# Kernel tuning notes

Measured on AMD Instinct MI355X. Metric: run time of the kernel, lower is better.

## Reference

```python
import jax, jax.numpy as jnp
import numpy as np

B, N, T, D, E, M = 8, 512, 64, 128, 32, 3


def _norm(v):
    return v / jnp.clip(jnp.linalg.norm(v, axis=-1, keepdims=True), 1e-12)


def setup_inputs() -> dict:
    key = jax.random.key(0)
    ks = jax.random.split(key, 14)
    s = 0.05
    x = jax.random.normal(ks[0], (B, N, T, 1), jnp.float32)
    # set_prior: binarized adjacency + self loops, row-normalized
    a = (jax.random.uniform(ks[1], (N, N)) > 0.95).astype(jnp.float32) + jnp.eye(N, dtype=jnp.float32)
    prior = a / jnp.clip(a.sum(1, keepdims=True), 1e-8)
    # orthogonal queries, as in torch __init__ (QR of zero-padded randn)
    rng = np.random.default_rng(0)
    qs = []
    for _ in range(M):
        pad = np.zeros((D, D), np.float32)
        pad[:E] = rng.standard_normal((E, D)).astype(np.float32) * 0.1
        q, _ = np.linalg.qr(pad)
        qs.append(q[:E])
    return {
        "x": x,
        "prior": prior,
        "proj_W": jax.random.normal(ks[2], (D, 1), jnp.float32) * s,
        "proj_b": jnp.zeros((D,), jnp.float32),
        "W_ih": jax.random.normal(ks[3], (3 * D, D), jnp.float32) * s,
        "W_hh": jax.random.normal(ks[4], (3 * D, D), jnp.float32) * s,
        "b_ih": jnp.zeros((3 * D,), jnp.float32),
        "b_hh": jnp.zeros((3 * D,), jnp.float32),
        "space_W": jax.random.normal(ks[5], (M, D, D), jnp.float32) * s,
        "space_b": jnp.zeros((M, D), jnp.float32),
        "router_W": jax.random.normal(ks[6], (M, 2 * D), jnp.float32) * s,
        "router_b": jnp.zeros((M,), jnp.float32),
        "out_W": jax.random.normal(ks[7], (1, D), jnp.float32) * s,
        "out_b": jnp.zeros((1,), jnp.float32),
        "prior_logit": jnp.array(1.0, jnp.float32),
        "queries": jnp.asarray(np.stack(qs)),  # [M, E, D]
    }


def reference(x, prior, proj_W, proj_b, W_ih, W_hh, b_ih, b_hh,
              space_W, space_b, router_W, router_b, out_W, out_b,
              prior_logit, queries):
    b, n, t, _ = x.shape
    d = proj_b.shape[0]
    m, e, _ = queries.shape
    # proj(x.permute(0,2,1,3)).reshape(B*N, T, D)  (faithful reshape of [B,T,N,D])
    hp = jnp.transpose(x, (0, 2, 1, 3)) @ proj_W.T + proj_b  # [B,T,N,D]
    seq = hp.reshape(b * n, t, d)
    xs = jnp.swapaxes(seq, 0, 1)  # [T, BN, D]

    def gru_step(h, xt):
        gi = xt @ W_ih.T + b_ih
        gh = h @ W_hh.T + b_hh
        ir, iz, i_n = jnp.split(gi, 3, axis=-1)
        hr, hz, h_n = jnp.split(gh, 3, axis=-1)
        r = jax.nn.sigmoid(ir + hr)
        z = jax.nn.sigmoid(iz + hz)
        ng = jnp.tanh(i_n + r * h_n)
        return (1.0 - z) * ng + z * h, None

    h, _ = jax.lax.scan(gru_step, jnp.zeros((b * n, d), x.dtype), xs)
    h = h.reshape(b, n, d)

    stats = jnp.concatenate([h.mean(1), jnp.std(h, axis=1, ddof=1)], axis=-1)  # torch std is unbiased
    probs = jax.nn.softmax(stats @ router_W.T + router_b, axis=-1)  # [B,M]

    z_prior = jnp.einsum('ij,bjd->bid', prior, h)

    hs = _norm(jnp.einsum('bnd,mkd->bmnk', h, space_W) + space_b[None, :, None, :])  # [B,M,N,D]
    q = _norm(queries)  # [M,E,D]
    scores = jnp.einsum('bmnd,med->bmen', hs, q)  # [B,M,E,N] (topk over N axis)
    k = min(n, max(4, int(n * 0.05)))
    vals, idx = jax.lax.top_k(scores, k)  # [B,M,E,k]
    w = jax.nn.softmax(vals / 0.7, axis=-1)
    H = jnp.zeros((b, m, e, n), h.dtype).at[
        jnp.arange(b)[:, None, None, None],
        jnp.arange(m)[None, :, None, None],
        jnp.arange(e)[None, None, :, None],
        idx,
    ].set(w)  # [B,M,E,N], transposed layout of torch's [B,N,E]

    Hmix = jnp.einsum('bmen,bm->ben', H, probs)  # [B,E,N] == torch Hmix^T
    edge = jnp.einsum('ben,bnd->bed', Hmix, h)   # Hmix^T @ h
    z_learn = jnp.einsum('ben,bed->bnd', Hmix, edge)  # Hmix @ edge

    alpha = jax.nn.sigmoid(prior_logit)
    out = (alpha * z_prior + (1.0 - alpha) * z_learn) @ out_W.T + out_b  # [B,N,1]
    return out.squeeze(-1), probs
```

## Files before the change

kernel.cpp:

```cpp
#include <hip/hip_runtime.h>
#include <math.h>

#define OFF_U      0
#define OFF_C      384
#define OFF_QWHI   768
#define OFF_QWLO   6912
#define OFF_H      13056
#define OFF_PROBS  537344
#define OFF_HV     537376
#define OFF_SCORES 541472
#define OFF_HMIX   934688
#define OFF_WHI    1066016
#define OFF_SHI    1115168
#define OFF_SLO    1139744
#define OFF_STATS  1164320
#define OFF_EV     1229856
#define OFF_QB     1230112

#define L2E_F 1.44269504088896340736f

typedef short bf16x8 __attribute__((ext_vector_type(8)));
typedef float f32x4 __attribute__((ext_vector_type(4)));

union U8 { unsigned short s[8]; bf16x8 v; uint4 u4; };

__device__ __forceinline__ unsigned short bf16_rtn(float f) {
  unsigned int u = __float_as_uint(f);
  return (unsigned short)((u + 0x7FFFu + ((u >> 16) & 1u)) >> 16);
}
__device__ __forceinline__ float bf16_f(unsigned short h) {
  return __uint_as_float(((unsigned int)h) << 16);
}

__global__ __launch_bounds__(256) void prep_kernel(const float* __restrict__ Wih,
                                                   const float* __restrict__ projW,
                                                   const float* __restrict__ projb,
                                                   const float* __restrict__ bih,
                                                   const float* __restrict__ queries,
                                                   const float* __restrict__ Whh,
                                                   const float* __restrict__ spaceW,
                                                   const float* __restrict__ spaceb,
                                                   float* __restrict__ ws) {
  const int bid = blockIdx.x, tid = threadIdx.x;
  const int wave = tid >> 6, lane = tid & 63;
  if (bid < 96) {
    int r = bid * 4 + wave;
    float w0 = Wih[r * 128 + lane], w1 = Wih[r * 128 + 64 + lane];
    float u = w0 * projW[lane] + w1 * projW[64 + lane];
    float c = w0 * projb[lane] + w1 * projb[64 + lane];
    for (int off = 32; off; off >>= 1) {
      u += __shfl_xor(u, off);
      c += __shfl_xor(c, off);
    }
    if (lane == 0) {
      ws[OFF_U + r] = u;
      ws[OFF_C + r] = c + bih[r];
    }
  } else if (bid < 112) {
    unsigned short* WHI = (unsigned short*)(ws + OFF_WHI);
    int base = (bid - 96) * 3072;
    for (int i = tid; i < 3072; i += 256) {
      int idx = base + i;
      float sc = (idx < 32768) ? L2E_F : (2.f * L2E_F);
      WHI[idx] = bf16_rtn(Whh[idx] * sc);
    }
  } else if (bid < 128) {
    unsigned short* SHI = (unsigned short*)(ws + OFF_SHI);
    unsigned short* SLO = (unsigned short*)(ws + OFF_SLO);
    int base = (bid - 112) * 3072;
    for (int i = tid; i < 3072; i += 256) {
      float w = spaceW[base + i];
      unsigned short hi = bf16_rtn(w);
      SHI[base + i] = hi;
      SLO[base + i] = bf16_rtn(w - bf16_f(hi));
    }
  } else if (bid < 224) {
    int qi = bid - 128;
    int m = qi >> 5, e = qi & 31;
    __shared__ float invS, qdS;
    const float* qrow = queries + (m * 32 + e) * 128;
    if (wave == 0) {
      float v0 = qrow[lane], v1 = qrow[64 + lane];
      float ss = v0 * v0 + v1 * v1;
      for (int off = 32; off; off >>= 1) ss += __shfl_xor(ss, off);
      if (lane == 0) invS = 1.f / fmaxf(sqrtf(ss), 1e-12f);
    } else if (wave == 1) {
      float v = qrow[lane] * spaceb[m * 128 + lane] +
                qrow[64 + lane] * spaceb[m * 128 + 64 + lane];
      for (int off = 32; off; off >>= 1) v += __shfl_xor(v, off);
      if (lane == 0) qdS = v;
    }
    __syncthreads();
    if (tid < 128) {
      int din = tid;
      float acc = 0.f;
      for (int dout = 0; dout < 128; ++dout)
        acc += qrow[dout] * spaceW[m * 16384 + dout * 128 + din];
      acc *= invS;
      unsigned short hi = bf16_rtn(acc);
      ((unsigned short*)(ws + OFF_QWHI))[(m * 32 + e) * 128 + din] = hi;
      ((unsigned short*)(ws + OFF_QWLO))[(m * 32 + e) * 128 + din] =
          bf16_rtn(acc - bf16_f(hi));
    }
    if (tid == 255) ws[OFF_QB + m * 32 + e] = qdS * invS;
  } else {
    ws[OFF_EV + tid] = 0.f;
  }
}

#define GRU_STEP(RB, WB, T)                                                         \
  do {                                                                              \
    f32x4 acc0 = c0i, acc1 = c1i, acc2 = c2i;                                       \
    _Pragma("unroll") for (int c = 0; c < 4; ++c) {                                 \
      bf16x8 Bf = *(const bf16x8*)&hB[RB][rdOff + c * 32];                          \
      acc0 = __builtin_amdgcn_mfma_f32_16x16x32_bf16(Ah[0][c], Bf, acc0, 0, 0, 0);  \
      acc1 = __builtin_amdgcn_mfma_f32_16x16x32_bf16(Ah[1][c], Bf, acc1, 0, 0, 0);  \
      acc2 = __builtin_amdgcn_mfma_f32_16x16x32_bf16(Ah[2][c], Bf, acc2, 0, 0, 0);  \
    }                                                                               \
    const float xsv = xsAll[xsOff + (T)];                                           \
    float hv[4];                                                                    \
    _Pragma("unroll") for (int r = 0; r < 4; ++r) {                                 \
      float gr = fmaf(xsv, ur[r], acc0[r]);                                         \
      float gz = fmaf(xsv, uz[r], acc1[r]);                                         \
      float gn = fmaf(xsv, un[r], cnv[r]);                                          \
      float rr = __builtin_amdgcn_rcpf(1.f + __builtin_amdgcn_exp2f(-gr));          \
      float zm = __builtin_amdgcn_rcpf(1.f + __builtin_amdgcn_exp2f(gz));           \
      float a = fmaf(rr, acc2[r], gn);                                              \
      float ng = fmaf(-2.f, __builtin_amdgcn_rcpf(__builtin_amdgcn_exp2f(a) + 1.f), \
                      1.f);                                                         \
      hv[r] = fmaf(zm, ng - hreg[r], hreg[r]);                                      \
      hreg[r] = hv[r];                                                              \
    }                                                                               \
    unsigned int pk0, pk1;                                                          \
    asm("v_cvt_pk_bf16_f32 %0, %1, %2" : "=v"(pk0) : "v"(hv[0]), "v"(hv[1]));       \
    asm("v_cvt_pk_bf16_f32 %0, %1, %2" : "=v"(pk1) : "v"(hv[2]), "v"(hv[3]));       \
    *(uint2*)&hB[WB][wrOff] = make_uint2(pk0, pk1);                                 \
    __syncthreads();                                                                \
  } while (0)

__global__ __launch_bounds__(512, 2) void gru_kernel(const float* __restrict__ x,
                                                     const float* __restrict__ bhh,
                                                     const float* __restrict__ outW,
                                                     float* __restrict__ ws) {
  __shared__ __align__(16) unsigned short hB[2][16 * 136];
  __shared__ float xsAll[16 * 65];
  __shared__ float hFin[16 * 132];

  const int tid = threadIdx.x, wave = tid >> 6, lane = tid & 63;
  const int q = lane >> 4, s15 = lane & 15;
  const int d0 = wave * 16 + q * 4;
  const unsigned short* WHI = (const unsigned short*)(ws + OFF_WHI);

  {
    float4 z4 = make_float4(0.f, 0.f, 0.f, 0.f);
    float4* hm4 = (float4*)(ws + OFF_HMIX);
    if (tid < 128) hm4[blockIdx.x * 128 + tid] = z4;
  }

  bf16x8 Ah[3][4];
#pragma unroll
  for (int t = 0; t < 3; ++t) {
    int row = (wave + 8 * t) * 16 + s15;
#pragma unroll
    for (int c = 0; c < 4; ++c)
      Ah[t][c] = *(const bf16x8*)&WHI[row * 128 + c * 32 + q * 8];
  }

  float ur[4], uz[4], un[4], cnv[4];
  f32x4 c0i, c1i, c2i;
#pragma unroll
  for (int r = 0; r < 4; ++r) {
    int d = d0 + r;
    ur[r] = ws[OFF_U + d] * L2E_F;
    uz[r] = ws[OFF_U + 128 + d] * L2E_F;
    un[r] = ws[OFF_U + 256 + d] * (2.f * L2E_F);
    c0i[r] = (ws[OFF_C + d] + bhh[d]) * L2E_F;
    c1i[r] = (ws[OFF_C + 128 + d] + bhh[128 + d]) * L2E_F;
    cnv[r] = ws[OFF_C + 256 + d] * (2.f * L2E_F);
    c2i[r] = bhh[256 + d] * (2.f * L2E_F);
  }

  const int seq0 = blockIdx.x * 16;
  for (int i = tid; i < 1024; i += 512) {
    int s = i >> 6, tt = i & 63;
    int r = (seq0 + s) * 64 + tt;
    xsAll[s * 65 + tt] = x[((r >> 15) * 512 + (r & 511)) * 64 + ((r >> 9) & 63)];
  }
  for (int i = tid; i < 2176; i += 512) hB[0][i] = 0;
  __syncthreads();

  float hreg[4] = {0.f, 0.f, 0.f, 0.f};
  const int rdOff = s15 * 136 + q * 8;
  const int wrOff = s15 * 136 + d0;
  const int xsOff = s15 * 65;

#pragma unroll 1
  for (int t2 = 0; t2 < 32; ++t2) {
    GRU_STEP(0, 1, 2 * t2);
    GRU_STEP(1, 0, 2 * t2 + 1);
  }

#pragma unroll
  for (int r = 0; r < 4; ++r) hFin[s15 * 132 + d0 + r] = hreg[r];
  __syncthreads();
  float* h_out = ws + OFF_H;
#pragma unroll
  for (int p = 0; p < 4; ++p) {
    int item = tid + p * 512;
    int s = item >> 7, dd = item & 127;
    h_out[(seq0 + s) * 128 + dd] = hFin[s * 132 + dd];
  }
  for (int s = wave * 2; s < wave * 2 + 2; ++s) {
    float a = hFin[s * 132 + lane] * outW[lane] + hFin[s * 132 + 64 + lane] * outW[64 + lane];
    for (int off = 32; off; off >>= 1) a += __shfl_xor(a, off);
    if (lane == 0) ws[OFF_HV + seq0 + s] = a;
  }
  if (tid < 128) {
    float s = 0.f, q2 = 0.f;
#pragma unroll
    for (int sI = 0; sI < 16; ++sI) {
      float v = hFin[sI * 132 + tid];
      s += v; q2 += v * v;
    }
    ws[OFF_STATS + blockIdx.x * 256 + tid] = s;
    ws[OFF_STATS + blockIdx.x * 256 + 128 + tid] = q2;
  }
}

__global__ __launch_bounds__(256) void scores_kernel(const float* __restrict__ spaceb,
                                                     const float* __restrict__ routerW,
                                                     const float* __restrict__ routerb,
                                                     float* __restrict__ ws,
                                                     float* __restrict__ d_out) {
  const int bid = blockIdx.x;
  const int chunk = bid & 15, m = (bid >> 4) % 3, b = bid / 48;
  const int n0 = chunk * 32;
  const int tid = threadIdx.x, wave = tid >> 6, lane = tid & 63;
  const int q = lane >> 4, s15 = lane & 15;

  __shared__ __align__(16) unsigned short sHi[16 * 33 * 8];
  __shared__ __align__(16) unsigned short sLo[16 * 33 * 8];
  __shared__ float hsL[32 * 132];
  __shared__ float biasL[128];
  __shared__ float invnL[32];
  __shared__ float qbL[32];

  const float* hG = ws + OFF_H;
  const unsigned short* SHI = (const unsigned short*)(ws + OFF_SHI);
  const unsigned short* SLO = (const unsigned short*)(ws + OFF_SLO);
  const unsigned short* QWHI = (const unsigned short*)(ws + OFF_QWHI);
  const unsigned short* QWLO = (const unsigned short*)(ws + OFF_QWLO);

  if (tid < 128) biasL[tid] = spaceb[m * 128 + tid];
  else if (tid < 160) qbL[tid - 128] = ws[OFF_QB + m * 32 + (tid - 128)];
  {
    int nn = tid >> 3, kc = tid & 7;
    const float* row = &hG[(b * 512 + n0 + nn) * 128 + kc * 16];
    U8 ph0, pl0, ph1, pl1;
#pragma unroll
    for (int j = 0; j < 8; ++j) {
      float v = row[j];
      unsigned short hi = bf16_rtn(v);
      ph0.s[j] = hi; pl0.s[j] = bf16_rtn(v - bf16_f(hi));
    }
#pragma unroll
    for (int j = 0; j < 8; ++j) {
      float v = row[8 + j];
      unsigned short hi = bf16_rtn(v);
      ph1.s[j] = hi; pl1.s[j] = bf16_rtn(v - bf16_f(hi));
    }
    int g0 = kc * 2;
    *(uint4*)&sHi[(g0 * 33 + nn) * 8] = ph0.u4;
    *(uint4*)&sLo[(g0 * 33 + nn) * 8] = pl0.u4;
    *(uint4*)&sHi[((g0 + 1) * 33 + nn) * 8] = ph1.u4;
    *(uint4*)&sLo[((g0 + 1) * 33 + nn) * 8] = pl1.u4;
  }
  __syncthreads();

  const int nt = wave >> 1;
  const int half = wave & 1;
  const int dt0 = half * 4;
  f32x4 acc[4] = {{0.f,0.f,0.f,0.f},{0.f,0.f,0.f,0.f},{0.f,0.f,0.f,0.f},{0.f,0.f,0.f,0.f}};
  f32x4 accS = {0.f, 0.f, 0.f, 0.f};
#pragma unroll
  for (int c = 0; c < 4; ++c) {
    bf16x8 Ahi = *(const bf16x8*)&sHi[((c * 4 + q) * 33 + nt * 16 + s15) * 8];
    bf16x8 Alo = *(const bf16x8*)&sLo[((c * 4 + q) * 33 + nt * 16 + s15) * 8];
#pragma unroll
    for (int i = 0; i < 4; ++i) {
      int row = m * 16384 + ((dt0 + i) * 16 + s15) * 128 + c * 32 + q * 8;
      bf16x8 Bhi = *(const bf16x8*)&SHI[row];
      bf16x8 Blo = *(const bf16x8*)&SLO[row];
      acc[i] = __builtin_amdgcn_mfma_f32_16x16x32_bf16(Ahi, Bhi, acc[i], 0, 0, 0);
      acc[i] = __builtin_amdgcn_mfma_f32_16x16x32_bf16(Alo, Bhi, acc[i], 0, 0, 0);
      acc[i] = __builtin_amdgcn_mfma_f32_16x16x32_bf16(Ahi, Blo, acc[i], 0, 0, 0);
    }
    {
      int row = (m * 32 + half * 16 + s15) * 128 + c * 32 + q * 8;
      bf16x8 Qhi = *(const bf16x8*)&QWHI[row];
      bf16x8 Qlo = *(const bf16x8*)&QWLO[row];
      accS = __builtin_amdgcn_mfma_f32_16x16x32_bf16(Ahi, Qhi, accS, 0, 0, 0);
      accS = __builtin_amdgcn_mfma_f32_16x16x32_bf16(Alo, Qhi, accS, 0, 0, 0);
      accS = __builtin_amdgcn_mfma_f32_16x16x32_bf16(Ahi, Qlo, accS, 0, 0, 0);
    }
  }
#pragma unroll
  for (int i = 0; i < 4; ++i) {
    int dcol = (dt0 + i) * 16 + s15;
    float bb = biasL[dcol];
#pragma unroll
    for (int r = 0; r < 4; ++r)
      hsL[(nt * 16 + q * 4 + r) * 132 + dcol] = acc[i][r] + bb;
  }
  __syncthreads();

  {
    int n = tid >> 3, kc = tid & 7;
    float ss = 0.f;
#pragma unroll
    for (int d4 = 0; d4 < 4; ++d4) {
      float4 v = *(const float4*)&hsL[n * 132 + kc * 16 + d4 * 4];
      ss += v.x * v.x + v.y * v.y + v.z * v.z + v.w * v.w;
    }
    ss += __shfl_xor(ss, 1); ss += __shfl_xor(ss, 2); ss += __shfl_xor(ss, 4);
    if (kc == 0) invnL[n] = 1.f / fmaxf(sqrtf(ss), 1e-12f);
  }
  __syncthreads();

  {
    int e = half * 16 + s15;
    float qb = qbL[e];
    int nb = nt * 16 + q * 4;
    float4 o;
    o.x = (accS[0] + qb) * invnL[nb + 0];
    o.y = (accS[1] + qb) * invnL[nb + 1];
    o.z = (accS[2] + qb) * invnL[nb + 2];
    o.w = (accS[3] + qb) * invnL[nb + 3];
    *(float4*)&ws[OFF_SCORES + ((b * 3 + m) * 32 + e) * 512 + n0 + nb] = o;
  }

  if ((bid % 48) == 0) {
    __syncthreads();
    float* st = hsL;
    float* lgS = hsL + 256;
    if (tid < 128) {
      float s = 0.f, q2 = 0.f;
      const float* base = ws + OFF_STATS + b * 32 * 256;
      for (int j = 0; j < 32; ++j) {
        s += base[j * 256 + tid];
        q2 += base[j * 256 + 128 + tid];
      }
      float mean = s * (1.f / 512.f);
      float var = (q2 - 512.f * mean * mean) * (1.f / 511.f);
      st[tid] = mean;
      st[128 + tid] = sqrtf(fmaxf(var, 0.f));
    }
    __syncthreads();
    if (tid < 3) {
      float acc2 = routerb[tid];
      for (int k = 0; k < 256; ++k) acc2 += st[k] * routerW[tid * 256 + k];
      lgS[tid] = acc2;
    }
    __syncthreads();
    if (tid == 0) {
      float mx = fmaxf(lgS[0], fmaxf(lgS[1], lgS[2]));
      float e0 = expf(lgS[0] - mx), e1 = expf(lgS[1] - mx), e2 = expf(lgS[2] - mx);
      float inv = 1.f / (e0 + e1 + e2);
      ws[OFF_PROBS + b * 3 + 0] = e0 * inv;
      ws[OFF_PROBS + b * 3 + 1] = e1 * inv;
      ws[OFF_PROBS + b * 3 + 2] = e2 * inv;
      d_out[4096 + b * 3 + 0] = e0 * inv;
      d_out[4096 + b * 3 + 1] = e1 * inv;
      d_out[4096 + b * 3 + 2] = e2 * inv;
    }
  }
}

__global__ __launch_bounds__(256) void topk_kernel(float* __restrict__ ws) {
  const int row0 = blockIdx.x * 4;
  const int b = row0 / 96;
  const int tid = threadIdx.x, wave = tid >> 6, lane = tid & 63;
  __shared__ float hvL[512];
  hvL[tid] = ws[OFF_HV + b * 512 + tid];
  hvL[256 + tid] = ws[OFF_HV + b * 512 + 256 + tid];
  __syncthreads();

  int row = row0 + wave;
  int m = (row / 32) % 3, e = row & 31;
  const float* sc = ws + OFF_SCORES + row * 512;
  float prob = ws[OFF_PROBS + b * 3 + m];

  float v[8];
#pragma unroll
  for (int j = 0; j < 8; ++j) v[j] = sc[j * 64 + lane];

  float selv = 0.f; int seli = 0; float maxv = 0.f;
  for (int it = 0; it < 25; ++it) {
    float bv = v[0]; int bj = 0;
#pragma unroll
    for (int j = 1; j < 8; ++j)
      if (v[j] > bv) { bv = v[j]; bj = j; }
    int bidx = bj * 64 + lane;
    for (int off = 32; off; off >>= 1) {
      float ov = __shfl_xor(bv, off);
      int oi = __shfl_xor(bidx, off);
      if (ov > bv || (ov == bv && oi < bidx)) { bv = ov; bidx = oi; }
    }
    if (lane == (bidx & 63)) v[bidx >> 6] = -INFINITY;
    if (it == 0) maxv = bv;
    if (lane == it) { selv = bv; seli = bidx; }
  }
  float ex = (lane < 25) ? __expf((selv - maxv) * (1.f / 0.7f)) : 0.f;
  float den = ex;
  for (int off = 32; off; off >>= 1) den += __shfl_xor(den, off);
  float w = prob * ex / den;
  if (lane < 25)
    atomicAdd(&ws[OFF_HMIX + (b * 32 + e) * 512 + seli], w);
  float evc = (lane < 25) ? w * hvL[seli] : 0.f;
  for (int off = 32; off; off >>= 1) evc += __shfl_xor(evc, off);
  if (lane == 0) atomicAdd(&ws[OFF_EV + b * 32 + e], evc);
}

__global__ __launch_bounds__(512) void final_kernel(const float* __restrict__ prior,
                                                    const float* __restrict__ outb,
                                                    const float* __restrict__ plog,
                                                    float* __restrict__ ws,
                                                    float* __restrict__ d_out) {
  const int bid = blockIdx.x;
  const int b = bid >> 4, ch = bid & 15;
  const int tid = threadIdx.x, wave = tid >> 6, lane = tid & 63;
  __shared__ float hvL[512], evL[32];
  hvL[tid] = ws[OFF_HV + b * 512 + tid];
  if (tid < 32) evL[tid] = ws[OFF_EV + b * 32 + tid];
  __syncthreads();
  float alpha = 1.f / (1.f + expf(-plog[0]));
  float ob = outb[0];
#pragma unroll
  for (int i = 0; i < 4; ++i) {
    int n = ch * 32 + wave * 4 + i;
    const float* pr = prior + n * 512;
    float s1 = 0.f;
#pragma unroll
    for (int j = 0; j < 8; ++j) s1 += pr[j * 64 + lane] * hvL[j * 64 + lane];
    float s2 = 0.f;
    if (lane < 32) s2 = ws[OFF_HMIX + (b * 32 + lane) * 512 + n] * evL[lane];
    float a = alpha * s1 + (1.f - alpha) * s2;
    for (int off = 32; off; off >>= 1) a += __shfl_xor(a, off);
    if (lane == 0) d_out[b * 512 + n] = a + ob;
  }
}

extern "C" void kernel_launch(void* const* d_in, const int* in_sizes, int n_in,
                              void* d_out, int out_size, void* d_ws, size_t ws_size,
                              hipStream_t stream) {
  const float* x       = (const float*)d_in[0];
  const float* prior   = (const float*)d_in[1];
  const float* projW   = (const float*)d_in[2];
  const float* projb   = (const float*)d_in[3];
  const float* Wih     = (const float*)d_in[4];
  const float* Whh     = (const float*)d_in[5];
  const float* bih     = (const float*)d_in[6];
  const float* bhh     = (const float*)d_in[7];
  const float* spaceW  = (const float*)d_in[8];
  const float* spaceb  = (const float*)d_in[9];
  const float* routerW = (const float*)d_in[10];
  const float* routerb = (const float*)d_in[11];
  const float* outW    = (const float*)d_in[12];
  const float* outb    = (const float*)d_in[13];
  const float* plog    = (const float*)d_in[14];
  const float* queries = (const float*)d_in[15];
  float* ws  = (float*)d_ws;
  float* out = (float*)d_out;

  prep_kernel<<<225, 256, 0, stream>>>(Wih, projW, projb, bih, queries, Whh,
                                       spaceW, spaceb, ws);
  gru_kernel<<<256, 512, 0, stream>>>(x, bhh, outW, ws);
  scores_kernel<<<384, 256, 0, stream>>>(spaceb, routerW, routerb, ws, out);
  topk_kernel<<<192, 256, 0, stream>>>(ws);
  final_kernel<<<128, 512, 0, stream>>>(prior, outb, plog, ws, out);
}
```

Baseline: 167.1 us.

## Halve GRU block to 4 waves, each computing two 16-row tiles per step

The GRU kernel now runs with 256 threads (4 waves) instead of 512, and each wave handles two 16-column slices of the hidden state. It loads B fragments from LDS once per step and reuses them across both tiles. The aim is to cut barrier cost per recurrent step and the redundant LDS reads of h. In exchange each wave carries twice the register state (W_hh fragments, accumulators, constants) and runs a longer serial chain of MFMA and gate math per step, so the per-step critical path may grow.

```diff
diff --git a/kernel.cpp b/kernel.cpp
--- a/kernel.cpp
+++ b/kernel.cpp
@@ -108,37 +108,50 @@
   }
 }
 
-#define GRU_STEP(RB, WB, T)                                                         \
+#define GRU_MFMA3(G, a0, a1, a2)                                                    \
+  _Pragma("unroll") for (int c = 0; c < 4; ++c) {                                   \
+    a0 = __builtin_amdgcn_mfma_f32_16x16x32_bf16(Ah[0][G][c], Bf[c], a0, 0, 0, 0);  \
+    a1 = __builtin_amdgcn_mfma_f32_16x16x32_bf16(Ah[1][G][c], Bf[c], a1, 0, 0, 0);  \
+    a2 = __builtin_amdgcn_mfma_f32_16x16x32_bf16(Ah[2][G][c], Bf[c], a2, 0, 0, 0);  \
+  }
+
+#define GRU_GATES(WB, a0, a1, a2, UR, UZ, UN, CNV, HR, WOFF)                        \
   do {                                                                              \
-    f32x4 acc0 = c0i, acc1 = c1i, acc2 = c2i;                                       \
-    _Pragma("unroll") for (int c = 0; c < 4; ++c) {                                 \
-      bf16x8 Bf = *(const bf16x8*)&hB[RB][rdOff + c * 32];                          \
-      acc0 = __builtin_amdgcn_mfma_f32_16x16x32_bf16(Ah[0][c], Bf, acc0, 0, 0, 0);  \
-      acc1 = __builtin_amdgcn_mfma_f32_16x16x32_bf16(Ah[1][c], Bf, acc1, 0, 0, 0);  \
-      acc2 = __builtin_amdgcn_mfma_f32_16x16x32_bf16(Ah[2][c], Bf, acc2, 0, 0, 0);  \
-    }                                                                               \
-    const float xsv = xsAll[xsOff + (T)];                                           \
     float hv[4];                                                                    \
     _Pragma("unroll") for (int r = 0; r < 4; ++r) {                                 \
-      float gr = fmaf(xsv, ur[r], acc0[r]);                                         \
-      float gz = fmaf(xsv, uz[r], acc1[r]);                                         \
-      float gn = fmaf(xsv, un[r], cnv[r]);                                          \
+      float gr = fmaf(xsv, UR[r], a0[r]);                                           \
+      float gz = fmaf(xsv, UZ[r], a1[r]);                                           \
+      float gn = fmaf(xsv, UN[r], CNV[r]);                                          \
       float rr = __builtin_amdgcn_rcpf(1.f + __builtin_amdgcn_exp2f(-gr));          \
       float zm = __builtin_amdgcn_rcpf(1.f + __builtin_amdgcn_exp2f(gz));           \
-      float a = fmaf(rr, acc2[r], gn);                                              \
+      float a = fmaf(rr, a2[r], gn);                                                \
       float ng = fmaf(-2.f, __builtin_amdgcn_rcpf(__builtin_amdgcn_exp2f(a) + 1.f), \
                       1.f);                                                         \
-      hv[r] = fmaf(zm, ng - hreg[r], hreg[r]);                                      \
-      hreg[r] = hv[r];                                                              \
+      hv[r] = fmaf(zm, ng - HR[r], HR[r]);                                          \
+      HR[r] = hv[r];                                                                \
     }                                                                               \
     unsigned int pk0, pk1;                                                          \
     asm("v_cvt_pk_bf16_f32 %0, %1, %2" : "=v"(pk0) : "v"(hv[0]), "v"(hv[1]));       \
     asm("v_cvt_pk_bf16_f32 %0, %1, %2" : "=v"(pk1) : "v"(hv[2]), "v"(hv[3]));       \
-    *(uint2*)&hB[WB][wrOff] = make_uint2(pk0, pk1);                                 \
+    *(uint2*)&hB[WB][WOFF] = make_uint2(pk0, pk1);                                  \
+  } while (0)
+
+#define GRU_STEP(RB, WB, T)                                                         \
+  do {                                                                              \
+    f32x4 a0A = c0iA, a1A = c1iA, a2A = c2iA;                                       \
+    f32x4 a0B = c0iB, a1B = c1iB, a2B = c2iB;                                       \
+    bf16x8 Bf[4];                                                                   \
+    _Pragma("unroll") for (int c = 0; c < 4; ++c)                                   \
+      Bf[c] = *(const bf16x8*)&hB[RB][rdOff + c * 32];                              \
+    const float xsv = xsAll[xsOff + (T)];                                           \
+    GRU_MFMA3(0, a0A, a1A, a2A)                                                     \
+    GRU_GATES(WB, a0A, a1A, a2A, urA, uzA, unA, cnvA, hA, wrA);                     \
+    GRU_MFMA3(1, a0B, a1B, a2B)                                                     \
+    GRU_GATES(WB, a0B, a1B, a2B, urB, uzB, unB, cnvB, hBr, wrB);                    \
     __syncthreads();                                                                \
   } while (0)
 
-__global__ __launch_bounds__(512, 2) void gru_kernel(const float* __restrict__ x,
+__global__ __launch_bounds__(256, 1) void gru_kernel(const float* __restrict__ x,
                                                      const float* __restrict__ bhh,
                                                      const float* __restrict__ outW,
                                                      float* __restrict__ ws) {
@@ -148,7 +161,8 @@
 
   const int tid = threadIdx.x, wave = tid >> 6, lane = tid & 63;
   const int q = lane >> 4, s15 = lane & 15;
-  const int d0 = wave * 16 + q * 4;
+  const int dA = wave * 32 + q * 4;
+  const int dB = dA + 16;
   const unsigned short* WHI = (const unsigned short*)(ws + OFF_WHI);
 
   {
@@ -157,41 +171,53 @@
     if (tid < 128) hm4[blockIdx.x * 128 + tid] = z4;
   }
 
-  bf16x8 Ah[3][4];
-#pragma unroll
-  for (int t = 0; t < 3; ++t) {
-    int row = (wave + 8 * t) * 16 + s15;
-#pragma unroll
-    for (int c = 0; c < 4; ++c)
-      Ah[t][c] = *(const bf16x8*)&WHI[row * 128 + c * 32 + q * 8];
-  }
-
-  float ur[4], uz[4], un[4], cnv[4];
-  f32x4 c0i, c1i, c2i;
+  bf16x8 Ah[3][2][4];
+#pragma unroll
+  for (int g = 0; g < 3; ++g)
+#pragma unroll
+    for (int T = 0; T < 2; ++T) {
+      int row = g * 128 + wave * 32 + T * 16 + s15;
+#pragma unroll
+      for (int c = 0; c < 4; ++c)
+        Ah[g][T][c] = *(const bf16x8*)&WHI[row * 128 + c * 32 + q * 8];
+    }
+
+  float urA[4], uzA[4], unA[4], cnvA[4], urB[4], uzB[4], unB[4], cnvB[4];
+  f32x4 c0iA, c1iA, c2iA, c0iB, c1iB, c2iB;
 #pragma unroll
   for (int r = 0; r < 4; ++r) {
-    int d = d0 + r;
-    ur[r] = ws[OFF_U + d] * L2E_F;
-    uz[r] = ws[OFF_U + 128 + d] * L2E_F;
-    un[r] = ws[OFF_U + 256 + d] * (2.f * L2E_F);
-    c0i[r] = (ws[OFF_C + d] + bhh[d]) * L2E_F;
-    c1i[r] = (ws[OFF_C + 128 + d] + bhh[128 + d]) * L2E_F;
-    cnv[r] = ws[OFF_C + 256 + d] * (2.f * L2E_F);
-    c2i[r] = bhh[256 + d] * (2.f * L2E_F);
+    int d = dA + r;
+    urA[r] = ws[OFF_U + d] * L2E_F;
+    uzA[r] = ws[OFF_U + 128 + d] * L2E_F;
+    unA[r] = ws[OFF_U + 256 + d] * (2.f * L2E_F);
+    c0iA[r] = (ws[OFF_C + d] + bhh[d]) * L2E_F;
+    c1iA[r] = (ws[OFF_C + 128 + d] + bhh[128 + d]) * L2E_F;
+    cnvA[r] = ws[OFF_C + 256 + d] * (2.f * L2E_F);
+    c2iA[r] = bhh[256 + d] * (2.f * L2E_F);
+    d = dB + r;
+    urB[r] = ws[OFF_U + d] * L2E_F;
+    uzB[r] = ws[OFF_U + 128 + d] * L2E_F;
+    unB[r] = ws[OFF_U + 256 + d] * (2.f * L2E_F);
+    c0iB[r] = (ws[OFF_C + d] + bhh[d]) * L2E_F;
+    c1iB[r] = (ws[OFF_C + 128 + d] + bhh[128 + d]) * L2E_F;
+    cnvB[r] = ws[OFF_C + 256 + d] * (2.f * L2E_F);
+    c2iB[r] = bhh[256 + d] * (2.f * L2E_F);
   }
 
   const int seq0 = blockIdx.x * 16;
-  for (int i = tid; i < 1024; i += 512) {
+  for (int i = tid; i < 1024; i += 256) {
     int s = i >> 6, tt = i & 63;
     int r = (seq0 + s) * 64 + tt;
     xsAll[s * 65 + tt] = x[((r >> 15) * 512 + (r & 511)) * 64 + ((r >> 9) & 63)];
   }
-  for (int i = tid; i < 2176; i += 512) hB[0][i] = 0;
-  __syncthreads();
-
-  float hreg[4] = {0.f, 0.f, 0.f, 0.f};
+  for (int i = tid; i < 2176; i += 256) hB[0][i] = 0;
+  __syncthreads();
+
+  float hA[4] = {0.f, 0.f, 0.f, 0.f};
+  float hBr[4] = {0.f, 0.f, 0.f, 0.f};
   const int rdOff = s15 * 136 + q * 8;
-  const int wrOff = s15 * 136 + d0;
+  const int wrA = s15 * 136 + dA;
+  const int wrB = s15 * 136 + dB;
   const int xsOff = s15 * 65;
 
 #pragma unroll 1
@@ -201,16 +227,19 @@
   }
 
 #pragma unroll
-  for (int r = 0; r < 4; ++r) hFin[s15 * 132 + d0 + r] = hreg[r];
+  for (int r = 0; r < 4; ++r) {
+    hFin[s15 * 132 + dA + r] = hA[r];
+    hFin[s15 * 132 + dB + r] = hBr[r];
+  }
   __syncthreads();
   float* h_out = ws + OFF_H;
 #pragma unroll
-  for (int p = 0; p < 4; ++p) {
-    int item = tid + p * 512;
+  for (int p = 0; p < 8; ++p) {
+    int item = tid + p * 256;
     int s = item >> 7, dd = item & 127;
     h_out[(seq0 + s) * 128 + dd] = hFin[s * 132 + dd];
   }
-  for (int s = wave * 2; s < wave * 2 + 2; ++s) {
+  for (int s = wave * 4; s < wave * 4 + 4; ++s) {
     float a = hFin[s * 132 + lane] * outW[lane] + hFin[s * 132 + 64 + lane] * outW[64 + lane];
     for (int off = 32; off; off >>= 1) a += __shfl_xor(a, off);
     if (lane == 0) ws[OFF_HV + seq0 + s] = a;
@@ -474,7 +503,7 @@
 
   prep_kernel<<<225, 256, 0, stream>>>(Wih, projW, projb, bih, queries, Whh,
                                        spaceW, spaceb, ws);
-  gru_kernel<<<256, 512, 0, stream>>>(x, bhh, outW, ws);
+  gru_kernel<<<256, 256, 0, stream>>>(x, bhh, outW, ws);
   scores_kernel<<<384, 256, 0, stream>>>(spaceb, routerW, routerb, ws, out);
   topk_kernel<<<192, 256, 0, stream>>>(ws);
   final_kernel<<<128, 512, 0, stream>>>(prior, outb, plog, ws, out);
```

New measurement: 174.2 us. 1.04x slower.
